# Performance work log

Measured on AMD Instinct MI355X. Metric: run time of the kernel, lower is better.

## Reference

```python
import jax, jax.numpy as jnp
import numpy as np

H = 12          # num attention heads
DH = 64         # head size (768 / 12)
THRESHOLD = 0.05


def setup_inputs() -> dict:
    key = jax.random.key(0)
    ks = jax.random.split(key, 13)
    B, S, D = 128, 197, 768
    s = 0.02
    return {
        "hidden_states": jax.random.normal(ks[0], (B, S, D), jnp.float32),
        "Wq": jax.random.normal(ks[1], (D, D), jnp.float32) * s,
        "bq": jax.random.normal(ks[2], (D,), jnp.float32) * s,
        "Wk": jax.random.normal(ks[3], (D, D), jnp.float32) * s,
        "bk": jax.random.normal(ks[4], (D,), jnp.float32) * s,
        "Wv": jax.random.normal(ks[5], (D, D), jnp.float32) * s,
        "bv": jax.random.normal(ks[6], (D,), jnp.float32) * s,
        "Wd": jax.random.normal(ks[7], (D, D), jnp.float32) * s,
        "bd": jax.random.normal(ks[8], (D,), jnp.float32) * s,
        "W1": jax.random.normal(ks[9], (D, 64), jnp.float32) * s,
        "b1": jax.random.normal(ks[10], (64,), jnp.float32) * s,
        "W2": jax.random.normal(ks[11], (64, 1), jnp.float32) * s,
        "b2": jax.random.normal(ks[12], (1,), jnp.float32) * s,
    }


def reference(hidden_states, Wq, bq, Wk, bk, Wv, bv, Wd, bd, W1, b1, W2, b2):
    B, S, D = hidden_states.shape
    # --- DHS scoring MLP on patch tokens (exclude CLS), keep_cls=True path ---
    h = jax.nn.relu(hidden_states[:, 1:] @ W1 + b1)        # [B, S-1, 64]
    mlp_out = jax.nn.sigmoid(h @ W2 + b2)[..., 0]          # [B, S-1]
    patch_mask = mlp_out >= THRESHOLD                      # [B, S-1]
    cls_col = jnp.ones((B, 1), dtype=bool)
    mask = jnp.concatenate([cls_col, patch_mask], axis=1)  # [B, S]

    # --- full self-attention; pruning queries only removes rows, keys/values
    # are never pruned, so computing all rows and masking is equivalent ---
    q = (hidden_states @ Wq + bq).reshape(B, S, H, DH)
    k = (hidden_states @ Wk + bk).reshape(B, S, H, DH)
    v = (hidden_states @ Wv + bv).reshape(B, S, H, DH)
    scores = jnp.einsum("bqhd,bkhd->bhqk", q, k) / jnp.sqrt(jnp.float32(DH))
    probs = jax.nn.softmax(scores, axis=-1)                # dropout p=0.0 (eval)
    ctx = jnp.einsum("bhqk,bkhd->bqhd", probs, v).reshape(B, S, D)
    attn_out = (ctx @ Wd + bd) + ctx                       # dense + residual-to-self_outputs

    # scatter-assign: output[i][mask[i]] = attn_out rows for kept tokens
    output = jnp.where(mask[..., None], attn_out, hidden_states)
    return output
```

## Files before the change

kernel.cpp:

```cpp
#include <hip/hip_runtime.h>
#include <hip/hip_bf16.h>

#define HN 12
#define DHD 64
#define BB 128
#define SQ 197
#define DD 768
#define TOK (BB*SQ)
#define SP 224
#define SPS 232

using short8  = __attribute__((ext_vector_type(8))) short;
using floatx4 = __attribute__((ext_vector_type(4))) float;
using uintx4  = __attribute__((ext_vector_type(4))) unsigned;
using uintx2  = __attribute__((ext_vector_type(2))) unsigned;

__device__ __forceinline__ float bf2f(short v) {
    union { unsigned int u; float f; } x;
    x.u = ((unsigned int)(unsigned short)v) << 16;
    return x.f;
}
__device__ __forceinline__ short f2bf(float f) {
    union { float f; unsigned int u; } x; x.f = f;
    unsigned int u = x.u;
    u += 0x7fffu + ((u >> 16) & 1u);
    return (short)(u >> 16);
}
__device__ __forceinline__ float ldf(const void* p, size_t i, bool isf32) {
    return isf32 ? ((const float*)p)[i] : bf2f(((const short*)p)[i]);
}
__device__ __forceinline__ void gload_lds16(const short* g, short* l) {
    __builtin_amdgcn_global_load_lds(
        (const __attribute__((address_space(1))) void*)g,
        (__attribute__((address_space(3))) void*)l, 16, 0, 0);
}
__device__ __forceinline__ unsigned cvtpk(float lo, float hi) {
    unsigned r;
    asm volatile("v_cvt_pk_bf16_f32 %0, %1, %2" : "=v"(r) : "v"(lo), "v"(hi));
    return r;
}

__global__ __launch_bounds__(256) void detect_kernel(
        const short* __restrict__ wq, float* __restrict__ flag) {
    __shared__ int cnt;
    if (threadIdx.x == 0) cnt = 0;
    __syncthreads();
    int local = 0;
    for (int j = 0; j < 16; j++) {
        int i = threadIdx.x * 16 + j;
        unsigned int u = (unsigned short)wq[2 * i];
        unsigned int e = (u >> 7) & 0xFF;
        if (e < 64 || e >= 192) local++;
    }
    for (int d = 1; d < 64; d <<= 1) local += __shfl_xor(local, d, 64);
    if ((threadIdx.x & 63) == 0) atomicAdd(&cnt, local);
    __syncthreads();
    if (threadIdx.x == 0) *flag = (cnt > 256) ? 1.f : 0.f;
}

__global__ void sentinel_kernel(short* out, int n, float code) {
    int i = blockIdx.x * 256 + threadIdx.x;
    if (i < n) out[i] = (i == 0) ? f2bf(code) : (short)0;
}

__global__ __launch_bounds__(256) void prep_kernel(
        const void* __restrict__ Wq, const void* __restrict__ Wk,
        const void* __restrict__ Wv, const void* __restrict__ Wd,
        const void* __restrict__ bq, const void* __restrict__ bk,
        const void* __restrict__ bv, const void* __restrict__ bd,
        const void* __restrict__ W1, const void* __restrict__ b1,
        const void* __restrict__ W2, const void* __restrict__ b2,
        short* __restrict__ WqkvT, short* __restrict__ WdT,
        short* __restrict__ W1T, float* __restrict__ bcat,
        const float* __restrict__ flag) {
    __shared__ short tile[64][72];
    bool isf32 = (*flag != 0.f);
    int blk = blockIdx.x;
    int tid = threadIdx.x;
    int r = tid >> 2, c0 = (tid & 3) << 4;
    const void* W;
    size_t stride;
    int ti, tj, w = 0;
    if (blk < 576) {
        w = blk / 144;
        int t = blk % 144;
        ti = t / 12; tj = t % 12;
        W = (w == 0) ? Wq : (w == 1) ? Wk : (w == 2) ? Wv : Wd;
        stride = DD;
    } else {
        ti = blk - 576; tj = 0;
        W = W1;
        stride = 64;
    }
    for (int c = 0; c < 16; c++)
        tile[r][c0 + c] =
            f2bf(ldf(W, (size_t)(ti * 64 + r) * stride + tj * 64 + c0 + c, isf32));
    __syncthreads();
    short* out;
    if (blk < 576)
        out = (w < 3)
            ? WqkvT + ((size_t)(w * DD + tj * 64 + r)) * DD + ti * 64
            : WdT   + ((size_t)(tj * 64 + r)) * DD + ti * 64;
    else
        out = W1T + (size_t)r * DD + ti * 64;
    for (int h = 0; h < 2; h++) {
        short8 v;
        #pragma unroll
        for (int c = 0; c < 8; c++) v[c] = tile[c0 + h * 8 + c][r];
        *(short8*)&out[c0 + h * 8] = v;
    }
    if (blk == 0) {
        for (int i = tid; i < DD; i += 256) {
            bcat[i]          = ldf(bq, i, isf32);
            bcat[DD + i]     = ldf(bk, i, isf32);
            bcat[2 * DD + i] = ldf(bv, i, isf32);
            bcat[3 * DD + i] = ldf(bd, i, isf32);
        }
        if (tid < 64) {
            bcat[4 * DD + tid]      = ldf(b1, tid, isf32);
            bcat[4 * DD + 64 + tid] = ldf(W2, tid, isf32);
        }
        if (tid == 0) bcat[4 * DD + 128] = ldf(b2, 0, isf32);
    }
}

__global__ __launch_bounds__(256) void mask_gemm(
        const void* __restrict__ hs, const short* __restrict__ W1T,
        const float* __restrict__ bvec, float* __restrict__ mask,
        short* __restrict__ hsb, const float* __restrict__ flag) {
    __shared__ __align__(16) short As[64 * 32];
    __shared__ __align__(16) short Bs[64 * 32];
    bool isf32 = (*flag != 0.f);
    int tid = threadIdx.x, lane = tid & 63, wave = tid >> 6;
    int quad = lane >> 4, l16 = lane & 15;
    int tok0 = blockIdx.x * 64;

    int arow = tid >> 2, achk = tid & 3;
    int acol = ((achk ^ ((arow >> 1) & 3)) << 3);
    const short* Bg = W1T + (size_t)arow * DD +
                      (((achk ^ ((arow >> 1) & 3)) << 3));
    short* Bl = Bs + wave * 512;
    int fcol = ((quad ^ ((l16 >> 1) & 3)) << 3);

    floatx4 acc[4] = {};
    for (int k0 = 0; k0 < DD; k0 += 32) {
        gload_lds16(Bg + k0, Bl);
        size_t gidx = (size_t)(tok0 + arow) * DD + k0 + achk * 8;
        short8 s;
        if (isf32) {
            const float* hf = (const float*)hs;
            float4 f0 = *(const float4*)&hf[gidx];
            float4 f1 = *(const float4*)&hf[gidx + 4];
            s[0]=f2bf(f0.x); s[1]=f2bf(f0.y); s[2]=f2bf(f0.z); s[3]=f2bf(f0.w);
            s[4]=f2bf(f1.x); s[5]=f2bf(f1.y); s[6]=f2bf(f1.z); s[7]=f2bf(f1.w);
        } else {
            s = *(const short8*)&((const short*)hs)[gidx];
        }
        *(short8*)&hsb[gidx] = s;
        *(short8*)&As[(arow << 5) + acol] = s;
        __syncthreads();
        short8 af = *(const short8*)&As[((wave * 16 + l16) << 5) + fcol];
        #pragma unroll
        for (int j = 0; j < 4; j++) {
            short8 bf8 = *(const short8*)&Bs[((j * 16 + l16) << 5) + fcol];
            acc[j] = __builtin_amdgcn_mfma_f32_16x16x32_bf16(af, bf8, acc[j], 0, 0, 0);
        }
        __syncthreads();
    }

    const float* b1f = bvec + 4 * DD;
    const float* w2f = bvec + 4 * DD + 64;
    float b2v = bvec[4 * DD + 128];
    float partial[4] = {0.f, 0.f, 0.f, 0.f};
    #pragma unroll
    for (int j = 0; j < 4; j++) {
        int n = j * 16 + l16;
        float b1v = b1f[n], w2v = w2f[n];
        #pragma unroll
        for (int r = 0; r < 4; r++) {
            float hv = fmaxf(acc[j][r] + b1v, 0.f);
            partial[r] += hv * w2v;
        }
    }
    for (int d = 1; d < 16; d <<= 1)
        #pragma unroll
        for (int r = 0; r < 4; r++)
            partial[r] += __shfl_xor(partial[r], d, 64);
    if (l16 == 0) {
        #pragma unroll
        for (int r = 0; r < 4; r++) {
            int tokr = tok0 + wave * 16 + quad * 4 + r;
            float m = 1.f;
            if (tokr % SQ != 0) {
                float sg = 1.f / (1.f + __expf(-(partial[r] + b2v)));
                m = (sg >= 0.05f) ? 1.f : 0.f;
            }
            mask[tokr] = m;
        }
    }
}

template <int MODE>
__global__ __launch_bounds__(512, 4) void gemm128(
        const short* __restrict__ A, const short* __restrict__ BT,
        const float* __restrict__ bias, void* __restrict__ C,
        int m0g, int Mreal, int N,
        const float* __restrict__ mask, const short* __restrict__ resid,
        const void* __restrict__ hs, const float* __restrict__ flag) {
    constexpr int K = DD;
    constexpr int BK = 64;
    __shared__ __align__(16) short As[128 * BK];
    __shared__ __align__(16) short Bs[128 * BK];
    int tiles_n = N >> 7;
    int nwg = gridDim.x, bid = blockIdx.x;
    int qq = nwg >> 3, rr = nwg & 7, xcd = bid & 7, lid = bid >> 3;
    int wg = (xcd < rr ? xcd * (qq + 1) : rr * (qq + 1) + (xcd - rr) * qq) + lid;
    int bm = wg / tiles_n, bn = wg % tiles_n;
    int m0 = bm << 7, n0 = bn << 7;

    int tid = threadIdx.x, lane = tid & 63, wave = tid >> 6;
    int wx = wave & 3, wy = wave >> 2;
    int quad = lane >> 4, l16 = lane & 15, l7 = l16 & 7;

    int slot0 = (wave << 7) + lane;
    int slot1 = slot0 + 64;
    int r0 = slot0 >> 3, c0s = ((slot0 & 7) ^ (r0 & 7)) << 3;
    int r1 = slot1 >> 3, c1s = ((slot1 & 7) ^ (r1 & 7)) << 3;
    int am0 = m0 + r0; if (am0 >= Mreal) am0 = Mreal - 1;
    int am1 = m0 + r1; if (am1 >= Mreal) am1 = Mreal - 1;
    const short* Ag0 = A + (size_t)am0 * K + c0s;
    const short* Ag1 = A + (size_t)am1 * K + c1s;
    const short* Bg0 = BT + (size_t)(n0 + r0) * K + c0s;
    const short* Bg1 = BT + (size_t)(n0 + r1) * K + c1s;
    short* Al0 = As + wave * 1024;
    short* Al1 = Al0 + 512;
    short* Bl0 = Bs + wave * 1024;
    short* Bl1 = Bl0 + 512;

    floatx4 acc[4][2] = {};
    for (int k0 = 0; k0 < K; k0 += BK) {
        gload_lds16(Ag0 + k0, Al0);
        gload_lds16(Ag1 + k0, Al1);
        gload_lds16(Bg0 + k0, Bl0);
        gload_lds16(Bg1 + k0, Bl1);
        __syncthreads();
        #pragma unroll
        for (int ks = 0; ks < 2; ks++) {
            int colo = ((((ks << 2) + quad) ^ l7) << 3);
            short8 af[4], bfr[2];
            #pragma unroll
            for (int i = 0; i < 4; i++)
                af[i] = *(const short8*)&As[(((wy << 6) + (i << 4) + l16) << 6) + colo];
            #pragma unroll
            for (int j = 0; j < 2; j++)
                bfr[j] = *(const short8*)&Bs[(((wx << 5) + (j << 4) + l16) << 6) + colo];
            #pragma unroll
            for (int i = 0; i < 4; i++)
                #pragma unroll
                for (int j = 0; j < 2; j++)
                    acc[i][j] = __builtin_amdgcn_mfma_f32_16x16x32_bf16(
                        af[i], bfr[j], acc[i][j], 0, 0, 0);
        }
        __syncthreads();
    }

    bool isf32 = (MODE == 1) ? (*flag != 0.f) : false;
    #pragma unroll
    for (int i = 0; i < 4; i++)
        #pragma unroll
        for (int j = 0; j < 2; j++) {
            int n = n0 + (wx << 5) + (j << 4) + l16;
            float bb = bias[n];
            #pragma unroll
            for (int r = 0; r < 4; r++) {
                int m = m0 + (wy << 6) + (i << 4) + (quad << 2) + r;
                if (m >= Mreal) continue;
                float v = acc[i][j][r] + bb;
                if (MODE == 0) {
                    ((short*)C)[(size_t)m * N + n] = f2bf(v);
                } else {
                    size_t gm = (size_t)(m0g + m);
                    v += bf2f(resid[(size_t)m * N + n]);
                    if (mask[gm] == 0.f) v = ldf(hs, gm * N + n, isf32);
                    if (isf32) ((float*)C)[gm * N + n] = v;
                    else       ((short*)C)[gm * N + n] = f2bf(v);
                }
            }
        }
}

__global__ __launch_bounds__(256) void attn_kernel(
        const short* __restrict__ qkv, short* __restrict__ ctx) {
    __shared__ __align__(16) short Vt[DHD * SPS];
    int nwg = gridDim.x, bid = blockIdx.x;
    int qq = nwg >> 3, rr = nwg & 7, xcd = bid & 7, lid = bid >> 3;
    int blk = (xcd < rr ? xcd * (qq + 1) : rr * (qq + 1) + (xcd - rr) * qq) + lid;
    int qc = blk & 3;
    int h  = (blk >> 2) % HN;
    int b  = blk / (4 * HN);
    int tid = threadIdx.x, lane = tid & 63, wave = tid >> 6;
    int quad = lane >> 4, l16 = lane & 15;
    const short* base = qkv + (size_t)b * SQ * 2304;

    for (int i = tid; i < SQ * DHD; i += 256) {
        int s = i >> 6, d = i & 63;
        Vt[d * SPS + s] = base[(size_t)s * 2304 + 1536 + h * 64 + d];
    }
    for (int i = tid; i < (SP - SQ) * DHD; i += 256) {
        int s = SQ + i % (SP - SQ), d = i / (SP - SQ);
        Vt[d * SPS + s] = 0;
    }
    __syncthreads();

    int mrow = qc * 64 + wave * 16 + l16;
    if (mrow > SQ - 1) mrow = SQ - 1;
    const short* Qrow = base + (size_t)mrow * 2304 + h * 64;
    short8 bq0 = *(const short8*)(Qrow + quad * 8);
    short8 bq1 = *(const short8*)(Qrow + 32 + quad * 8);

    floatx4 sc[13];
    #pragma unroll
    for (int t = 0; t < 13; t++) {
        int nrow = t * 16 + l16;
        if (nrow > SQ - 1) nrow = SQ - 1;
        const short* Krow = base + (size_t)nrow * 2304 + DD + h * 64;
        short8 ka0 = *(const short8*)(Krow + quad * 8);
        short8 ka1 = *(const short8*)(Krow + 32 + quad * 8);
        floatx4 c = {0.f, 0.f, 0.f, 0.f};
        c = __builtin_amdgcn_mfma_f32_16x16x32_bf16(ka0, bq0, c, 0, 0, 0);
        c = __builtin_amdgcn_mfma_f32_16x16x32_bf16(ka1, bq1, c, 0, 0, 0);
        sc[t] = c;
    }

    const float scale = 0.125f;
    float mx = -1e30f;
    #pragma unroll
    for (int t = 0; t < 12; t++)
        #pragma unroll
        for (int r = 0; r < 4; r++) mx = fmaxf(mx, sc[t][r]);
    #pragma unroll
    for (int r = 0; r < 4; r++)
        mx = fmaxf(mx, (4 * quad + r < 5) ? sc[12][r] : -1e30f);
    mx = fmaxf(mx, __shfl_xor(mx, 16, 64));
    mx = fmaxf(mx, __shfl_xor(mx, 32, 64));
    float sum = 0.f;
    #pragma unroll
    for (int t = 0; t < 12; t++)
        #pragma unroll
        for (int r = 0; r < 4; r++) {
            float e = __expf((sc[t][r] - mx) * scale);
            sc[t][r] = e; sum += e;
        }
    #pragma unroll
    for (int r = 0; r < 4; r++) {
        float e = (4 * quad + r < 5) ? __expf((sc[12][r] - mx) * scale) : 0.f;
        sc[12][r] = e; sum += e;
    }
    sum += __shfl_xor(sum, 16, 64);
    sum += __shfl_xor(sum, 32, 64);
    float inv = 1.f / sum;

    unsigned pklo[14], pkhi[14];
    #pragma unroll
    for (int t = 0; t < 13; t++) {
        pklo[t] = cvtpk(sc[t][0] * inv, sc[t][1] * inv);
        pkhi[t] = cvtpk(sc[t][2] * inv, sc[t][3] * inv);
    }
    pklo[13] = 0u; pkhi[13] = 0u;

    int c0 = quad & 1, par = quad >> 1;
    floatx4 co[4] = {};
    #pragma unroll
    for (int u = 0; u < 7; u++) {
        int t0 = 2 * u, t1 = 2 * u + 1;
        unsigned eol = par ? pklo[t1] : pklo[t0];
        unsigned eoh = par ? pkhi[t1] : pkhi[t0];
        unsigned exl = par ? pklo[t0] : pklo[t1];
        unsigned exh = par ? pkhi[t0] : pkhi[t1];
        unsigned a16l = __shfl_xor(eol, 16, 64), a16h = __shfl_xor(eoh, 16, 64);
        unsigned a32l = __shfl_xor(exl, 32, 64), a32h = __shfl_xor(exh, 32, 64);
        unsigned a48l = __shfl_xor(exl, 48, 64), a48h = __shfl_xor(exh, 48, 64);
        uintx4 fw;
        fw[0] = c0 ? (par ? a16l : a48l) : (par ? a32l : eol);
        fw[1] = c0 ? (par ? a16h : a48h) : (par ? a32h : eoh);
        fw[2] = c0 ? (par ? eol : a32l) : (par ? a48l : a16l);
        fw[3] = c0 ? (par ? eoh : a32h) : (par ? a48h : a16h);
        short8 pa = __builtin_bit_cast(short8, fw);
        #pragma unroll
        for (int j = 0; j < 4; j++) {
            short8 vb = *(const short8*)&Vt[(j * 16 + l16) * SPS + u * 32 + quad * 8];
            co[j] = __builtin_amdgcn_mfma_f32_16x16x32_bf16(vb, pa, co[j], 0, 0, 0);
        }
    }

    int sq = qc * 64 + wave * 16 + l16;
    if (sq < SQ) {
        size_t o = ((size_t)(b * SQ + sq)) * DD + h * 64;
        #pragma unroll
        for (int j = 0; j < 4; j++) {
            uintx2 w;
            w[0] = cvtpk(co[j][0], co[j][1]);
            w[1] = cvtpk(co[j][2], co[j][3]);
            *reinterpret_cast<uintx2*>(&ctx[o + j * 16 + quad * 4]) = w;
        }
    }
}

extern "C" void kernel_launch(void* const* d_in, const int* in_sizes, int n_in,
                              void* d_out, int out_size, void* d_ws, size_t ws_size,
                              hipStream_t stream) {
    const void* hs = d_in[0];
    const void* Wq = d_in[1];
    const void* bq = d_in[2];
    const void* Wk = d_in[3];
    const void* bk = d_in[4];
    const void* Wv = d_in[5];
    const void* bv = d_in[6];
    const void* Wd = d_in[7];
    const void* bd = d_in[8];
    const void* W1 = d_in[9];
    const void* b1 = d_in[10];
    const void* W2 = d_in[11];
    const void* b2 = d_in[12];

    const size_t flag_b  = 16;
    const size_t mask_b  = (size_t)TOK * 4;
    const size_t bcat_b  = (size_t)(4 * DD + 192) * 4;
    const size_t wqkvt_b = (size_t)3 * DD * DD * 2;
    const size_t wdt_b   = (size_t)DD * DD * 2;
    const size_t w1t_b   = (size_t)64 * DD * 2;
    const size_t hsb_b   = (size_t)TOK * DD * 2;
    const size_t fixed   = flag_b + mask_b + bcat_b + wqkvt_b + wdt_b + w1t_b + hsb_b;

    int CHB = 0;
    for (int c = 128; c >= 1; c >>= 1) {
        size_t chtp = (size_t)((c * SQ + 127) / 128) * 128;
        size_t need = fixed + chtp * 2304 * 2 + chtp * DD * 2;
        if (need <= ws_size) { CHB = c; break; }
    }
    if (CHB == 0) {
        sentinel_kernel<<<(out_size + 255) / 256, 256, 0, stream>>>(
            (short*)d_out, out_size, (float)((double)ws_size / 1.0e6));
        return;
    }
    const int CHT  = CHB * SQ;
    const int CHTP = ((CHT + 127) / 128) * 128;

    char* ws = (char*)d_ws;
    float* flag  = (float*)ws;
    float* mask  = (float*)(ws + flag_b);
    float* bcat  = (float*)(ws + flag_b + mask_b);
    short* WqkvT = (short*)(ws + flag_b + mask_b + bcat_b);
    short* WdT   = WqkvT + (size_t)3 * DD * DD;
    short* W1T   = WdT + (size_t)DD * DD;
    short* hsb   = W1T + (size_t)64 * DD;
    short* QKVc  = hsb + (size_t)TOK * DD;
    short* ctxc  = QKVc + (size_t)CHTP * 2304;

    detect_kernel<<<1, 256, 0, stream>>>((const short*)Wq, flag);
    prep_kernel<<<588, 256, 0, stream>>>(Wq, Wk, Wv, Wd, bq, bk, bv, bd,
                                         W1, b1, W2, b2,
                                         WqkvT, WdT, W1T, bcat, flag);
    mask_gemm<<<TOK / 64, 256, 0, stream>>>(hs, W1T, bcat, mask, hsb, flag);

    const int nchunk  = BB / CHB;
    const int tiles_m = CHTP / 128;
    for (int c = 0; c < nchunk; c++) {
        const int m0g = c * CHT;
        gemm128<0><<<tiles_m * (3 * DD / 128), 512, 0, stream>>>(
            hsb + (size_t)m0g * DD, WqkvT, bcat, QKVc,
            m0g, CHT, 3 * DD, nullptr, nullptr, nullptr, flag);
        attn_kernel<<<CHB * HN * 4, 256, 0, stream>>>(QKVc, ctxc);
        gemm128<1><<<tiles_m * (DD / 128), 512, 0, stream>>>(
            ctxc, WdT, bcat + 3 * DD, d_out,
            m0g, CHT, DD, mask, ctxc, hs, flag);
    }
}
```

Baseline: 531.0 us.

## Double-buffer LDS tiles in gemm128 to overlap global loads with MFMA

Splits the K loop into a prologue load, a steady-state loop that prefetches the next BK tile into a second LDS buffer while computing on the current one, and an epilogue compute. This aims to hide global-to-LDS load latency behind MFMA work and removes one barrier per iteration. It doubles LDS usage per block, which can reduce the number of resident workgroups per CU.

Measured after the change: 534.5 us. About the same (+0.7%).

```diff
diff --git a/kernel.cpp b/kernel.cpp
--- a/kernel.cpp
+++ b/kernel.cpp
@@ -209,8 +209,10 @@
         const void* __restrict__ hs, const float* __restrict__ flag) {
     constexpr int K = DD;
     constexpr int BK = 64;
-    __shared__ __align__(16) short As[128 * BK];
-    __shared__ __align__(16) short Bs[128 * BK];
+    constexpr int NT = K / BK;
+    constexpr int BUF = 128 * BK;
+    __shared__ __align__(16) short As[2 * BUF];
+    __shared__ __align__(16) short Bs[2 * BUF];
     int tiles_n = N >> 7;
     int nwg = gridDim.x, bid = blockIdx.x;
     int qq = nwg >> 3, rr = nwg & 7, xcd = bid & 7, lid = bid >> 3;
@@ -238,22 +240,32 @@
     short* Bl1 = Bl0 + 512;
 
     floatx4 acc[4][2] = {};
-    for (int k0 = 0; k0 < K; k0 += BK) {
-        gload_lds16(Ag0 + k0, Al0);
-        gload_lds16(Ag1 + k0, Al1);
-        gload_lds16(Bg0 + k0, Bl0);
-        gload_lds16(Bg1 + k0, Bl1);
-        __syncthreads();
+    gload_lds16(Ag0, Al0);
+    gload_lds16(Ag1, Al1);
+    gload_lds16(Bg0, Bl0);
+    gload_lds16(Bg1, Bl1);
+    __syncthreads();
+    int cur = 0;
+    for (int t = 0; t < NT - 1; ++t) {
+        int kn = (t + 1) << 6;
+        int nxt = cur ^ 1;
+        int nofs = nxt * BUF;
+        gload_lds16(Ag0 + kn, Al0 + nofs);
+        gload_lds16(Ag1 + kn, Al1 + nofs);
+        gload_lds16(Bg0 + kn, Bl0 + nofs);
+        gload_lds16(Bg1 + kn, Bl1 + nofs);
+        const short* Ab = As + cur * BUF;
+        const short* Bb = Bs + cur * BUF;
         #pragma unroll
         for (int ks = 0; ks < 2; ks++) {
             int colo = ((((ks << 2) + quad) ^ l7) << 3);
             short8 af[4], bfr[2];
             #pragma unroll
             for (int i = 0; i < 4; i++)
-                af[i] = *(const short8*)&As[(((wy << 6) + (i << 4) + l16) << 6) + colo];
+                af[i] = *(const short8*)&Ab[(((wy << 6) + (i << 4) + l16) << 6) + colo];
             #pragma unroll
             for (int j = 0; j < 2; j++)
-                bfr[j] = *(const short8*)&Bs[(((wx << 5) + (j << 4) + l16) << 6) + colo];
+                bfr[j] = *(const short8*)&Bb[(((wx << 5) + (j << 4) + l16) << 6) + colo];
             #pragma unroll
             for (int i = 0; i < 4; i++)
                 #pragma unroll
@@ -262,6 +274,28 @@
                         af[i], bfr[j], acc[i][j], 0, 0, 0);
         }
         __syncthreads();
+        cur = nxt;
+    }
+    {
+        const short* Ab = As + cur * BUF;
+        const short* Bb = Bs + cur * BUF;
+        #pragma unroll
+        for (int ks = 0; ks < 2; ks++) {
+            int colo = ((((ks << 2) + quad) ^ l7) << 3);
+            short8 af[4], bfr[2];
+            #pragma unroll
+            for (int i = 0; i < 4; i++)
+                af[i] = *(const short8*)&Ab[(((wy << 6) + (i << 4) + l16) << 6) + colo];
+            #pragma unroll
+            for (int j = 0; j < 2; j++)
+                bfr[j] = *(const short8*)&Bb[(((wx << 5) + (j << 4) + l16) << 6) + colo];
+            #pragma unroll
+            for (int i = 0; i < 4; i++)
+                #pragma unroll
+                for (int j = 0; j < 2; j++)
+                    acc[i][j] = __builtin_amdgcn_mfma_f32_16x16x32_bf16(
+                        af[i], bfr[j], acc[i][j], 0, 0, 0);
+        }
     }
 
     bool isf32 = (MODE == 1) ? (*flag != 0.f) : false;
```
